# Kernel optimization log

Hardware: AMD Instinct MI355X
Metric: run time of the kernel (lower is better)

## Reference

```python
import jax, jax.numpy as jnp
import numpy as np

EMBED_DIM = 768
NUM_HEADS = 12
HEAD_DIM = EMBED_DIM // NUM_HEADS
SCALE = HEAD_DIM ** -0.5


def setup_inputs() -> dict:
    key = jax.random.key(0)
    k_x, k_wqkv, k_bqkv, k_wfc, k_bfc = jax.random.split(key, 5)
    B, S, D = 32, 577, EMBED_DIM
    x = jax.random.normal(k_x, (B, S, D), dtype=jnp.float32)
    # torch Linear default init ~ U(-1/sqrt(fan_in), 1/sqrt(fan_in)); scale suffices
    lim = 1.0 / np.sqrt(D)
    w_qkv = jax.random.uniform(k_wqkv, (D, 3 * D), jnp.float32, -lim, lim)
    b_qkv = jax.random.uniform(k_bqkv, (3 * D,), jnp.float32, -lim, lim)
    w_fc = jax.random.uniform(k_wfc, (D, D), jnp.float32, -lim, lim)
    b_fc = jax.random.uniform(k_bfc, (D,), jnp.float32, -lim, lim)
    return {"x": x, "w_qkv": w_qkv, "b_qkv": b_qkv, "w_fc": w_fc, "b_fc": b_fc}


def reference(x, w_qkv, b_qkv, w_fc, b_fc):
    B, S, D = x.shape
    H, Dh = NUM_HEADS, HEAD_DIM
    qkv = x @ w_qkv + b_qkv                      # [B,S,3D]
    qkv = qkv.reshape(B, S, 3, H, Dh)
    q, k, v = jnp.moveaxis(qkv, 2, 0)            # each [B,S,H,Dh]
    # scores: [B,H,S,S]
    attn = jnp.einsum('bqhd,bkhd->bhqk', q, k) * SCALE
    attn = jax.nn.softmax(attn, axis=-1)
    out = jnp.einsum('bhqk,bkhd->bqhd', attn, v).reshape(B, S, D)
    # dropout in eval mode -> identity
    return out @ w_fc + b_fc
```

## Files before the change

### kernel.cpp

```cpp
#include <hip/hip_runtime.h>
#include <hip/hip_bf16.h>
#include <stdint.h>

typedef __attribute__((ext_vector_type(8))) short short8;
typedef __attribute__((ext_vector_type(4))) float f32x4;

typedef __attribute__((address_space(3))) uint8_t lds_u8;
typedef __attribute__((address_space(1))) uint8_t glb_u8;

__device__ __forceinline__ void load_lds_16(const void* g, void* l) {
    __builtin_amdgcn_global_load_lds((glb_u8*)g, (lds_u8*)l, 16, 0, 0);
}

__device__ __forceinline__ unsigned short f2b(float f) {
    __hip_bfloat16 h = __float2bfloat16(f);
    return __builtin_bit_cast(unsigned short, h);
}
__device__ __forceinline__ ushort2 f2b2(float a, float b) {
    __hip_bfloat162 h = __float22bfloat162_rn(float2{a, b});
    ushort2 r;
    __builtin_memcpy(&r, &h, sizeof(r));
    return r;
}
__device__ __forceinline__ float b2f(unsigned short u) {
    unsigned int x = ((unsigned int)u) << 16;
    return __builtin_bit_cast(float, x);
}

constexpr int Bz = 32, Ss = 577, Dd = 768, Hh = 12;
constexpr int Mm = Bz * Ss;
constexpr int QKV_N = 3 * Dd;
constexpr float SCALE_L2E = 0.125f * 1.4426950408889634f;

__global__ void cast_f32_bf16(const float* __restrict__ src,
                              unsigned short* __restrict__ dst, int n4) {
    int i = blockIdx.x * blockDim.x + threadIdx.x;
    if (i >= n4) return;
    float4 v = ((const float4*)src)[i];
    ushort4 o;
    o.x = f2b(v.x); o.y = f2b(v.y); o.z = f2b(v.z); o.w = f2b(v.w);
    ((ushort4*)dst)[i] = o;
}

__global__ void transpose_cast(const float* __restrict__ src,
                               unsigned short* __restrict__ dst, int R, int C) {
    __shared__ unsigned short tile[32][33];
    int c0 = blockIdx.x * 32, r0 = blockIdx.y * 32;
    int tx = threadIdx.x, ty = threadIdx.y;
#pragma unroll
    for (int i = 0; i < 4; ++i)
        tile[ty + i * 8][tx] = f2b(src[(size_t)(r0 + ty + i * 8) * C + c0 + tx]);
    __syncthreads();
#pragma unroll
    for (int i = 0; i < 4; ++i) {
        int rr = ty + i * 8;
        dst[(size_t)(c0 + rr) * R + r0 + tx] = tile[tx][rr];
    }
}

template <int N_, bool OUT_BF16>
__global__ __launch_bounds__(512, 2)
void gemm256(const unsigned short* __restrict__ A,
             const unsigned short* __restrict__ Bt,
             const float* __restrict__ bias,
             void* __restrict__ Cout) {
    constexpr int K = 768;
    constexpr int KB = 12;
    constexpr int NX = N_ / 256;
    constexpr int NY = (Mm + 255) / 256;
    constexpr int NWG = NX * NY;
    constexpr int QC = NWG >> 3, RC = NWG & 7;
    extern __shared__ __align__(16) uint8_t smem[];

    const int tid = threadIdx.x;
    const int wave = tid >> 6, lane = tid & 63;
    const int quad = lane >> 4, lc = lane & 15;
    const int wm = wave >> 2, wn = wave & 3;

    const int orig = blockIdx.y * NX + blockIdx.x;
    const int xcd = orig & 7, lid = orig >> 3;
    const int wgid = (xcd < RC ? xcd * (QC + 1) : RC * (QC + 1) + (xcd - RC) * QC) + lid;
    const int tm = (wgid / NX) * 256;
    const int tn = (wgid % NX) * 256;

    const int colsw = ((lane & 7) ^ (lane >> 3)) * 8;
    const unsigned short* rpA[2][2];
    const unsigned short* rpB[2][2];
#pragma unroll
    for (int s = 0; s < 2; ++s) {
        const int prs = (s * 8 + wave) * 8 + (lane >> 3);
#pragma unroll
        for (int h = 0; h < 2; ++h) {
            int ar = tm + (prs >> 6) * 128 + h * 64 + (prs & 63);
            if (ar >= Mm) ar = Mm - 1;
            rpA[s][h] = A + (size_t)ar * K + colsw;
            int br = tn + (prs >> 5) * 64 + h * 32 + (prs & 31);
            rpB[s][h] = Bt + (size_t)br * K + colsw;
        }
    }

    auto ldsA = [&](int b, int mh) -> uint8_t* { return smem + b * 65536 + mh * 16384; };
    auto ldsB = [&](int b, int nh) -> uint8_t* { return smem + b * 65536 + 32768 + nh * 16384; };

    auto stageA = [&](int kb, int mh) {
        uint8_t* d = ldsA(kb & 1, mh) + wave * 1024;
        load_lds_16(rpA[0][mh] + kb * 64, d);
        load_lds_16(rpA[1][mh] + kb * 64, d + 8192);
    };
    auto stageB = [&](int kb, int nh) {
        uint8_t* d = ldsB(kb & 1, nh) + wave * 1024;
        load_lds_16(rpB[0][nh] + kb * 64, d);
        load_lds_16(rpB[1][nh] + kb * 64, d + 8192);
    };

    short8 af[2][4], bf[2][2];
    auto readA = [&](int b, int mh) {
        const unsigned short* p = (const unsigned short*)ldsA(b, mh);
#pragma unroll
        for (int i = 0; i < 4; ++i) {
            const int pr = wm * 64 + i * 16 + lc;
            const unsigned short* r = p + pr * 64;
            const int sw = pr & 7;
            af[0][i] = *(const short8*)(r + ((quad) ^ sw) * 8);
            af[1][i] = *(const short8*)(r + ((4 + quad) ^ sw) * 8);
        }
    };
    auto readB = [&](int b, int nh) {
        const unsigned short* p = (const unsigned short*)ldsB(b, nh);
#pragma unroll
        for (int j = 0; j < 2; ++j) {
            const int pr = wn * 32 + j * 16 + lc;
            const unsigned short* r = p + pr * 64;
            const int sw = pr & 7;
            bf[0][j] = *(const short8*)(r + ((quad) ^ sw) * 8);
            bf[1][j] = *(const short8*)(r + ((4 + quad) ^ sw) * 8);
        }
    };

    f32x4 acc[8][4] = {};
    auto quadmfma = [&](int mh, int nh) {
        __builtin_amdgcn_s_setprio(1);
#pragma unroll
        for (int ks = 0; ks < 2; ++ks)
#pragma unroll
            for (int i = 0; i < 4; ++i)
#pragma unroll
                for (int j = 0; j < 2; ++j)
                    acc[mh * 4 + i][nh * 2 + j] = __builtin_amdgcn_mfma_f32_16x16x32_bf16(
                        af[ks][i], bf[ks][j], acc[mh * 4 + i][nh * 2 + j], 0, 0, 0);
        __builtin_amdgcn_s_setprio(0);
    };

    stageA(0, 0); stageA(0, 1); stageB(0, 0); stageB(0, 1);
    asm volatile("s_waitcnt vmcnt(0)" ::: "memory");
    __builtin_amdgcn_s_barrier();
    __builtin_amdgcn_sched_barrier(0);

    for (int T = 0; T < KB; ++T) {
        const int rb = T & 1;
        readA(rb, 0);
        readB(rb, 0);
        if (T + 1 < KB) {
            stageA(T + 1, 0); stageA(T + 1, 1);
            stageB(T + 1, 0); stageB(T + 1, 1);
        }
        quadmfma(0, 0);
        readB(rb, 1);
        quadmfma(0, 1);
        readA(rb, 1);
        quadmfma(1, 1);
        readB(rb, 0);
        quadmfma(1, 0);
        asm volatile("s_waitcnt vmcnt(0)" ::: "memory");
        __builtin_amdgcn_s_barrier();
        __builtin_amdgcn_sched_barrier(0);
    }

    float bv[4];
#pragma unroll
    for (int j = 0; j < 4; ++j) bv[j] = bias[tn + wn * 64 + j * 16 + lc];

    float* ep = (float*)smem + wave * (16 * 68);
    const int erow = lane >> 2, ec = (lane & 3) * 16;
#pragma unroll
    for (int ia = 0; ia < 8; ++ia) {
#pragma unroll
        for (int j = 0; j < 4; ++j)
#pragma unroll
            for (int r = 0; r < 4; ++r)
                ep[(quad * 4 + r) * 68 + j * 16 + lc] = acc[ia][j][r] + bv[j];
        __threadfence_block();
        int grow = tm + wm * 128 + ia * 16 + erow;
        if (grow < Mm) {
            float4 c0 = *(float4*)&ep[erow * 68 + ec + 0];
            float4 c1 = *(float4*)&ep[erow * 68 + ec + 4];
            float4 c2 = *(float4*)&ep[erow * 68 + ec + 8];
            float4 c3 = *(float4*)&ep[erow * 68 + ec + 12];
            int gcol = tn + wn * 64 + ec;
            if constexpr (OUT_BF16) {
                unsigned short o[16];
                *(ushort2*)&o[0]  = f2b2(c0.x, c0.y);
                *(ushort2*)&o[2]  = f2b2(c0.z, c0.w);
                *(ushort2*)&o[4]  = f2b2(c1.x, c1.y);
                *(ushort2*)&o[6]  = f2b2(c1.z, c1.w);
                *(ushort2*)&o[8]  = f2b2(c2.x, c2.y);
                *(ushort2*)&o[10] = f2b2(c2.z, c2.w);
                *(ushort2*)&o[12] = f2b2(c3.x, c3.y);
                *(ushort2*)&o[14] = f2b2(c3.z, c3.w);
                unsigned short* op = (unsigned short*)Cout + (size_t)grow * N_ + gcol;
                *(short8*)(op + 0) = *(short8*)&o[0];
                *(short8*)(op + 8) = *(short8*)&o[8];
            } else {
                float* op = (float*)Cout + (size_t)grow * N_ + gcol;
                *(float4*)(op + 0)  = c0;
                *(float4*)(op + 4)  = c1;
                *(float4*)(op + 8)  = c2;
                *(float4*)(op + 12) = c3;
            }
        }
        __threadfence_block();
    }
}

__device__ __forceinline__ void attn_tile(
    const unsigned short* __restrict__ Ktile,
    const unsigned short* __restrict__ Vtb,
    unsigned short* __restrict__ Pqw,
    const short8& qf0, const short8& qf1,
    int quad, int lc,
    f32x4 (&oacc)[4], f32x4& lacc) {

    const int sw = lc & 7;
    f32x4 sfr[4];
    __builtin_amdgcn_s_setprio(1);
#pragma unroll
    for (int f = 0; f < 4; ++f) {
        const unsigned short* kr = Ktile + (f * 16 + lc) * 64;
        short8 k0 = *(const short8*)(kr + (quad ^ sw) * 8);
        short8 k1 = *(const short8*)(kr + ((quad ^ 4) ^ sw) * 8);
        f32x4 z = {};
        z = __builtin_amdgcn_mfma_f32_16x16x32_bf16(k0, qf0, z, 0, 0, 0);
        z = __builtin_amdgcn_mfma_f32_16x16x32_bf16(k1, qf1, z, 0, 0, 0);
        sfr[f] = z;
    }
    __builtin_amdgcn_s_setprio(0);

#pragma unroll
    for (int f = 0; f < 4; ++f) {
        float p[4];
#pragma unroll
        for (int r = 0; r < 4; ++r)
            p[r] = __builtin_amdgcn_exp2f(sfr[f][r] * SCALE_L2E);
        ushort2 lo = f2b2(p[0], p[1]), hi = f2b2(p[2], p[3]);
        ushort4 pk = {lo.x, lo.y, hi.x, hi.y};
        *(ushort4*)&Pqw[lc * 72 + f * 16 + quad * 4] = pk;
    }

    __threadfence_block();

    short8 pf0 = *(const short8*)&Pqw[lc * 72 + quad * 8];
    short8 pf1 = *(const short8*)&Pqw[lc * 72 + 32 + quad * 8];
    __builtin_amdgcn_s_setprio(1);
#pragma unroll
    for (int g = 0; g < 4; ++g) {
        short8 vf0 = *(const short8*)&Vtb[(g * 16 + lc) * 80 + quad * 8];
        short8 vf1 = *(const short8*)&Vtb[(g * 16 + lc) * 80 + 32 + quad * 8];
        oacc[g] = __builtin_amdgcn_mfma_f32_16x16x32_bf16(vf0, pf0, oacc[g], 0, 0, 0);
        oacc[g] = __builtin_amdgcn_mfma_f32_16x16x32_bf16(vf1, pf1, oacc[g], 0, 0, 0);
    }
    short8 vo0 = *(const short8*)&Vtb[(64 + lc) * 80 + quad * 8];
    short8 vo1 = *(const short8*)&Vtb[(64 + lc) * 80 + 32 + quad * 8];
    lacc = __builtin_amdgcn_mfma_f32_16x16x32_bf16(vo0, pf0, lacc, 0, 0, 0);
    lacc = __builtin_amdgcn_mfma_f32_16x16x32_bf16(vo1, pf1, lacc, 0, 0, 0);
    __builtin_amdgcn_s_setprio(0);
}

__global__ __launch_bounds__(512)
void attn_kernel(const unsigned short* __restrict__ qkv,
                 unsigned short* __restrict__ outb) {
    __shared__ unsigned short Kt[2][64 * 64];
    __shared__ unsigned short Vt[2][80 * 80];
    __shared__ unsigned short Pq[8][16 * 72];

    const int tid = threadIdx.x;
    const int wave = tid >> 6, lane = tid & 63;
    const int quad = lane >> 4, lc = lane & 15;

    const int orig = (blockIdx.z * gridDim.y + blockIdx.y) * gridDim.x + blockIdx.x;
    const int wgid = (orig & 7) * 240 + (orig >> 3);
    const int qt = wgid % 5;
    const int h  = (wgid / 5) % Hh;
    const int b  = wgid / (5 * Hh);

    const unsigned short* qkvK = qkv + (size_t)b * Ss * QKV_N + h * 64 + 768;
    const unsigned short* qkvV = qkvK + 768;

    const int krow = lane >> 3;
    const int gch = (lane & 7) ^ krow;

    const int qbase = qt * 128 + wave * 16;
    int qrow = qbase + lc; if (qrow > Ss - 1) qrow = Ss - 1;
    const unsigned short* qp = qkv + (size_t)(b * Ss + qrow) * QKV_N + h * 64;
    short8 qf0 = *(const short8*)(qp + quad * 8);
    short8 qf1 = *(const short8*)(qp + 32 + quad * 8);

    unsigned short* Pqw = Pq[wave];

    auto stage_K = [&](int tile, int buf) {
        int key = tile * 64 + wave * 8 + krow;
        const unsigned short* gp = qkvK + (size_t)key * QKV_N + gch * 8;
        load_lds_16(gp, (void*)&Kt[buf][wave * 512]);
    };
    auto load_V = [&](int tile) -> short8 {
        int key = tile * 64 + lane;
        return *(const short8*)(qkvV + (size_t)key * QKV_N + wave * 8);
    };
    auto write_V = [&](short8 v, int buf) {
#pragma unroll
        for (int j = 0; j < 8; ++j)
            Vt[buf][(wave * 8 + j) * 80 + lane] = (unsigned short)v[j];
    };

    if (tid < 80) {
        Vt[0][64 * 80 + tid] = 0x3F80;
        Vt[1][64 * 80 + tid] = 0x3F80;
    }

    f32x4 oacc[4] = {};
    f32x4 lacc = {};

    stage_K(0, 0);
    write_V(load_V(0), 0);
    __syncthreads();

    for (int kb = 0; kb < 8; ++kb) {
        const int buf = kb & 1;
        stage_K(kb + 1, buf ^ 1);
        short8 vreg = load_V(kb + 1);
        attn_tile(Kt[buf], Vt[buf], Pqw, qf0, qf1, quad, lc, oacc, lacc);
        write_V(vreg, buf ^ 1);
        __syncthreads();
    }
    attn_tile(Kt[0], Vt[0], Pqw, qf0, qf1, quad, lc, oacc, lacc);

    float ptail;
    {
        const unsigned short* k576 = qkvK + (size_t)576 * QKV_N;
        short8 kk0 = *(const short8*)(k576 + quad * 8);
        short8 kk1 = *(const short8*)(k576 + 32 + quad * 8);
        float part = 0.f;
#pragma unroll
        for (int j = 0; j < 8; ++j)
            part += b2f((unsigned short)qf0[j]) * b2f((unsigned short)kk0[j])
                  + b2f((unsigned short)qf1[j]) * b2f((unsigned short)kk1[j]);
        part += __shfl_xor(part, 16, 64);
        part += __shfl_xor(part, 32, 64);
        ptail = __builtin_amdgcn_exp2f(part * SCALE_L2E);
        const unsigned short* v576 = qkvV + (size_t)576 * QKV_N;
#pragma unroll
        for (int g = 0; g < 4; ++g) {
            ushort4 vv = *(const ushort4*)(v576 + g * 16 + quad * 4);
            oacc[g][0] += ptail * b2f(vv.x);
            oacc[g][1] += ptail * b2f(vv.y);
            oacc[g][2] += ptail * b2f(vv.z);
            oacc[g][3] += ptail * b2f(vv.w);
        }
    }

    float lq = __shfl(lacc[0], lc, 64) + ptail;
    float inv = 1.f / lq;
#pragma unroll
    for (int g = 0; g < 4; ++g) {
        ushort2 lo = f2b2(oacc[g][0] * inv, oacc[g][1] * inv);
        ushort2 hi = f2b2(oacc[g][2] * inv, oacc[g][3] * inv);
        ushort4 ob = {lo.x, lo.y, hi.x, hi.y};
        *(ushort4*)&Pqw[lc * 72 + g * 16 + quad * 4] = ob;
    }
    __threadfence_block();
#pragma unroll
    for (int p = 0; p < 2; ++p) {
        int lr = p * 8 + (lane >> 3), ch = lane & 7;
        int q = qbase + lr;
        if (q <= Ss - 1) {
            short8 vv = *(const short8*)&Pqw[lr * 72 + ch * 8];
            *(short8*)(outb + (size_t)(b * Ss + q) * Dd + h * 64 + ch * 8) = vv;
        }
    }
}

extern "C" void kernel_launch(void* const* d_in, const int* in_sizes, int n_in,
                              void* d_out, int out_size, void* d_ws, size_t ws_size,
                              hipStream_t stream) {
    const float* x     = (const float*)d_in[0];
    const float* w_qkv = (const float*)d_in[1];
    const float* b_qkv = (const float*)d_in[2];
    const float* w_fc  = (const float*)d_in[3];
    const float* b_fc  = (const float*)d_in[4];

    uint8_t* ws = (uint8_t*)d_ws;
    unsigned short* xb    = (unsigned short*)(ws + 0);
    unsigned short* wqkvT = (unsigned short*)(ws + 28360704);
    unsigned short* wfcT  = (unsigned short*)(ws + 31899648);
    unsigned short* qkv   = (unsigned short*)(ws + 33079296);
    unsigned short* attn  = (unsigned short*)(ws + 118161408);

    static bool lds_init = false;
    if (!lds_init) {
        hipFuncSetAttribute((const void*)gemm256<QKV_N, true>,
                            hipFuncAttributeMaxDynamicSharedMemorySize, 131072);
        hipFuncSetAttribute((const void*)gemm256<Dd, false>,
                            hipFuncAttributeMaxDynamicSharedMemorySize, 131072);
        lds_init = true;
    }

    int n4 = (Mm * Dd) / 4;
    cast_f32_bf16<<<(n4 + 255) / 256, 256, 0, stream>>>(x, xb, n4);
    transpose_cast<<<dim3(QKV_N / 32, Dd / 32), dim3(32, 8), 0, stream>>>(w_qkv, wqkvT, Dd, QKV_N);
    transpose_cast<<<dim3(Dd / 32, Dd / 32), dim3(32, 8), 0, stream>>>(w_fc, wfcT, Dd, Dd);

    gemm256<QKV_N, true><<<dim3(QKV_N / 256, (Mm + 255) / 256), 512, 131072, stream>>>(xb, wqkvT, b_qkv, qkv);

    attn_kernel<<<dim3(5, Hh, Bz), 512, 0, stream>>>(qkv, attn);

    gemm256<Dd, false><<<dim3(Dd / 256, (Mm + 255) / 256), 512, 131072, stream>>>(attn, wfcT, b_fc, d_out);
}
```

Baseline: 308.0 us.

## Restructure GEMM mainloop to triple-buffered K=32 stages with two-deep prefetch

The GEMM main loop changes from double-buffered 64-wide K blocks, which wait on all loads at every step, to a three-buffer ring of 32-wide K blocks. Two stages are kept in flight and the wait only drains older loads (vmcnt(4)). The LDS layout is repacked into 128-byte rows with a new XOR swizzle. Dynamic LDS drops from 128KB to 96KB. The aim is to hide global-to-LDS latency behind MFMAs, at the cost of twice as many barriers per K.

After: 312.3 us. Within noise of the previous version (+1.4%).

```diff
diff --git a/kernel.cpp b/kernel.cpp
--- a/kernel.cpp
+++ b/kernel.cpp
@@ -65,7 +65,7 @@
              const float* __restrict__ bias,
              void* __restrict__ Cout) {
     constexpr int K = 768;
-    constexpr int KB = 12;
+    constexpr int KB = 24;
     constexpr int NX = N_ / 256;
     constexpr int NY = (Mm + 255) / 256;
     constexpr int NWG = NX * NY;
@@ -83,98 +83,84 @@
     const int tm = (wgid / NX) * 256;
     const int tn = (wgid % NX) * 256;
 
-    const int colsw = ((lane & 7) ^ (lane >> 3)) * 8;
-    const unsigned short* rpA[2][2];
-    const unsigned short* rpB[2][2];
+    const int lrw = wave * 8 + (lane >> 3);
+    const unsigned short* apS[2];
+    const unsigned short* bpS[2];
 #pragma unroll
     for (int s = 0; s < 2; ++s) {
-        const int prs = (s * 8 + wave) * 8 + (lane >> 3);
-#pragma unroll
-        for (int h = 0; h < 2; ++h) {
-            int ar = tm + (prs >> 6) * 128 + h * 64 + (prs & 63);
-            if (ar >= Mm) ar = Mm - 1;
-            rpA[s][h] = A + (size_t)ar * K + colsw;
-            int br = tn + (prs >> 5) * 64 + h * 32 + (prs & 31);
-            rpB[s][h] = Bt + (size_t)br * K + colsw;
+        const int lr = s * 64 + lrw;
+        const int chun = (lane & 7) ^ (lr & 7);
+        const int trow = lr * 2 + (chun >> 2);
+        int ar = tm + trow; if (ar >= Mm) ar = Mm - 1;
+        apS[s] = A + (size_t)ar * K + (chun & 3) * 8;
+        const int br = tn + trow;
+        bpS[s] = Bt + (size_t)br * K + (chun & 3) * 8;
+    }
+
+    auto stage = [&](int kb, int buf) {
+        uint8_t* d = smem + buf * 32768 + wave * 1024;
+        const int ko = kb * 32;
+        load_lds_16(apS[0] + ko, d);
+        load_lds_16(apS[1] + ko, d + 8192);
+        load_lds_16(bpS[0] + ko, d + 16384);
+        load_lds_16(bpS[1] + ko, d + 24576);
+    };
+
+    const int slotS = (((lane & 1) << 2) + quad) ^ ((lc >> 1) & 7);
+    const int aoff = (wm * 64 + (lc >> 1)) * 128 + slotS * 16;
+    const int boff = 16384 + (wn * 32 + (lc >> 1)) * 128 + slotS * 16;
+
+    short8 af[8], bf[4];
+    auto readfr = [&](int buf) {
+        const uint8_t* p = smem + buf * 32768;
+#pragma unroll
+        for (int m = 0; m < 8; ++m) af[m] = *(const short8*)(p + aoff + m * 1024);
+#pragma unroll
+        for (int n = 0; n < 4; ++n) bf[n] = *(const short8*)(p + boff + n * 1024);
+    };
+
+    f32x4 acc[8][4] = {};
+    auto mfmas = [&]() {
+        __builtin_amdgcn_s_setprio(1);
+#pragma unroll
+        for (int m = 0; m < 8; ++m)
+#pragma unroll
+            for (int n = 0; n < 4; ++n)
+                acc[m][n] = __builtin_amdgcn_mfma_f32_16x16x32_bf16(af[m], bf[n], acc[m][n], 0, 0, 0);
+        __builtin_amdgcn_s_setprio(0);
+    };
+
+    stage(0, 0);
+    stage(1, 1);
+    asm volatile("s_waitcnt vmcnt(4)" ::: "memory");
+    __builtin_amdgcn_s_barrier();
+
+#pragma unroll 1
+    for (int t3 = 0; t3 < 7; ++t3) {
+        const int T = t3 * 3;
+#pragma unroll
+        for (int u = 0; u < 3; ++u) {
+            const int rb = u;
+            const int sb = (u + 2) % 3;
+            stage(T + u + 2, sb);
+            readfr(rb);
+            mfmas();
+            asm volatile("s_waitcnt vmcnt(4)" ::: "memory");
+            __builtin_amdgcn_s_barrier();
         }
     }
-
-    auto ldsA = [&](int b, int mh) -> uint8_t* { return smem + b * 65536 + mh * 16384; };
-    auto ldsB = [&](int b, int nh) -> uint8_t* { return smem + b * 65536 + 32768 + nh * 16384; };
-
-    auto stageA = [&](int kb, int mh) {
-        uint8_t* d = ldsA(kb & 1, mh) + wave * 1024;
-        load_lds_16(rpA[0][mh] + kb * 64, d);
-        load_lds_16(rpA[1][mh] + kb * 64, d + 8192);
-    };
-    auto stageB = [&](int kb, int nh) {
-        uint8_t* d = ldsB(kb & 1, nh) + wave * 1024;
-        load_lds_16(rpB[0][nh] + kb * 64, d);
-        load_lds_16(rpB[1][nh] + kb * 64, d + 8192);
-    };
-
-    short8 af[2][4], bf[2][2];
-    auto readA = [&](int b, int mh) {
-        const unsigned short* p = (const unsigned short*)ldsA(b, mh);
-#pragma unroll
-        for (int i = 0; i < 4; ++i) {
-            const int pr = wm * 64 + i * 16 + lc;
-            const unsigned short* r = p + pr * 64;
-            const int sw = pr & 7;
-            af[0][i] = *(const short8*)(r + ((quad) ^ sw) * 8);
-            af[1][i] = *(const short8*)(r + ((4 + quad) ^ sw) * 8);
-        }
-    };
-    auto readB = [&](int b, int nh) {
-        const unsigned short* p = (const unsigned short*)ldsB(b, nh);
-#pragma unroll
-        for (int j = 0; j < 2; ++j) {
-            const int pr = wn * 32 + j * 16 + lc;
-            const unsigned short* r = p + pr * 64;
-            const int sw = pr & 7;
-            bf[0][j] = *(const short8*)(r + ((quad) ^ sw) * 8);
-            bf[1][j] = *(const short8*)(r + ((4 + quad) ^ sw) * 8);
-        }
-    };
-
-    f32x4 acc[8][4] = {};
-    auto quadmfma = [&](int mh, int nh) {
-        __builtin_amdgcn_s_setprio(1);
-#pragma unroll
-        for (int ks = 0; ks < 2; ++ks)
-#pragma unroll
-            for (int i = 0; i < 4; ++i)
-#pragma unroll
-                for (int j = 0; j < 2; ++j)
-                    acc[mh * 4 + i][nh * 2 + j] = __builtin_amdgcn_mfma_f32_16x16x32_bf16(
-                        af[ks][i], bf[ks][j], acc[mh * 4 + i][nh * 2 + j], 0, 0, 0);
-        __builtin_amdgcn_s_setprio(0);
-    };
-
-    stageA(0, 0); stageA(0, 1); stageB(0, 0); stageB(0, 1);
+    stage(23, 2);
+    readfr(0);
+    mfmas();
+    asm volatile("s_waitcnt vmcnt(4)" ::: "memory");
+    __builtin_amdgcn_s_barrier();
+    readfr(1);
+    mfmas();
     asm volatile("s_waitcnt vmcnt(0)" ::: "memory");
     __builtin_amdgcn_s_barrier();
-    __builtin_amdgcn_sched_barrier(0);
-
-    for (int T = 0; T < KB; ++T) {
-        const int rb = T & 1;
-        readA(rb, 0);
-        readB(rb, 0);
-        if (T + 1 < KB) {
-            stageA(T + 1, 0); stageA(T + 1, 1);
-            stageB(T + 1, 0); stageB(T + 1, 1);
-        }
-        quadmfma(0, 0);
-        readB(rb, 1);
-        quadmfma(0, 1);
-        readA(rb, 1);
-        quadmfma(1, 1);
-        readB(rb, 0);
-        quadmfma(1, 0);
-        asm volatile("s_waitcnt vmcnt(0)" ::: "memory");
-        __builtin_amdgcn_s_barrier();
-        __builtin_amdgcn_sched_barrier(0);
-    }
+    readfr(2);
+    mfmas();
+    __builtin_amdgcn_s_barrier();
 
     float bv[4];
 #pragma unroll
@@ -407,9 +393,9 @@
     static bool lds_init = false;
     if (!lds_init) {
         hipFuncSetAttribute((const void*)gemm256<QKV_N, true>,
-                            hipFuncAttributeMaxDynamicSharedMemorySize, 131072);
+                            hipFuncAttributeMaxDynamicSharedMemorySize, 98304);
         hipFuncSetAttribute((const void*)gemm256<Dd, false>,
-                            hipFuncAttributeMaxDynamicSharedMemorySize, 131072);
+                            hipFuncAttributeMaxDynamicSharedMemorySize, 98304);
         lds_init = true;
     }
 
@@ -418,9 +404,9 @@
     transpose_cast<<<dim3(QKV_N / 32, Dd / 32), dim3(32, 8), 0, stream>>>(w_qkv, wqkvT, Dd, QKV_N);
     transpose_cast<<<dim3(Dd / 32, Dd / 32), dim3(32, 8), 0, stream>>>(w_fc, wfcT, Dd, Dd);
 
-    gemm256<QKV_N, true><<<dim3(QKV_N / 256, (Mm + 255) / 256), 512, 131072, stream>>>(xb, wqkvT, b_qkv, qkv);
+    gemm256<QKV_N, true><<<dim3(QKV_N / 256, (Mm + 255) / 256), 512, 98304, stream>>>(xb, wqkvT, b_qkv, qkv);
 
     attn_kernel<<<dim3(5, Hh, Bz), 512, 0, stream>>>(qkv, attn);
 
-    gemm256<Dd, false><<<dim3(Dd / 256, (Mm + 255) / 256), 512, 131072, stream>>>(attn, wfcT, b_fc, d_out);
-}
+    gemm256<Dd, false><<<dim3(Dd / 256, (Mm + 255) / 256), 512, 98304, stream>>>(attn, wfcT, b_fc, d_out);
+}
```
